# Performance work log

Measured on AMD Instinct MI355X. Metric: run time of the kernel, lower is better.

The kernel has to match this reference:

```python
import jax, jax.numpy as jnp
import numpy as np

GATE_INIT_BIAS = -0.6931471805599453  # -log(2)

def mish(x):
    return x * jnp.tanh(jax.nn.softplus(x))

def setup_inputs() -> dict:
    key = jax.random.key(0)
    ks = jax.random.split(key, 24)
    B = 262144
    x = jax.random.normal(ks[0], (B, 18), dtype=jnp.float32)
    band = jax.random.randint(ks[1], (B,), 0, 9).astype(jnp.float32)
    x = x.at[:, 17].set(band)
    def lin(k, fan_in, shape):
        bound = 1.0 / np.sqrt(fan_in)
        return jax.random.uniform(k, shape, jnp.float32, -bound, bound)
    inp = {
        'x': x,
        # trunk: 15->512->256 (Mish)
        'tw1': lin(ks[2], 15, (15, 512)),  'tb1': lin(ks[3], 15, (512,)),
        'tw2': lin(ks[4], 512, (512, 256)), 'tb2': lin(ks[5], 512, (256,)),
        # 9 band heads: 256->128->1, stacked on leading axis
        'hw1': lin(ks[6], 256, (9, 256, 128)), 'hb1': lin(ks[7], 256, (9, 128)),
        'hw2': lin(ks[8], 128, (9, 128)),      'hb2': lin(ks[9], 128, (9,)),
        # sun scaler head 256->64->1 (final layer zero weight, bias = gate_init_bias)
        'sw1': lin(ks[10], 256, (256, 64)), 'sb1': lin(ks[11], 256, (64,)),
        'sw2': jnp.zeros((64, 1), jnp.float32), 'sb2': jnp.full((1,), GATE_INIT_BIAS, jnp.float32),
        # storm scaler head
        'stw1': lin(ks[12], 256, (256, 64)), 'stb1': lin(ks[13], 256, (64,)),
        'stw2': jnp.zeros((64, 1), jnp.float32), 'stb2': jnp.full((1,), GATE_INIT_BIAS, jnp.float32),
        # monotonic sidecars: 1->8->1, softplus-positivized weights
        'sun_w1': lin(ks[14], 1, (1, 8)),  'sun_b1': lin(ks[15], 1, (8,)),
        'sun_w2': lin(ks[16], 8, (8, 1)),  'sun_b2': lin(ks[17], 8, (1,)),
        'storm_w1': lin(ks[18], 1, (1, 8)), 'storm_b1': lin(ks[19], 1, (8,)),
        'storm_w2': lin(ks[20], 8, (8, 1)), 'storm_b2': lin(ks[21], 8, (1,)),
    }
    return inp

def monotonic_mlp(v, w1, b1, w2, b2):
    # MonotonicMLP: positivity via softplus on weights, tanh hidden activation
    h = jnp.tanh(v @ jax.nn.softplus(w1) + b1)
    return h @ jax.nn.softplus(w2) + b2  # [B,1]

def reference(x, tw1, tb1, tw2, tb2, hw1, hb1, hw2, hb2,
              sw1, sb1, sw2, sb2, stw1, stb1, stw2, stb2,
              sun_w1, sun_b1, sun_w2, sun_b2,
              storm_w1, storm_b1, storm_w2, storm_b2):
    x_deep = x[:, :15]
    x_sfi = x[:, 15:16]
    x_kp = x[:, 16:17]
    band = x[:, 17].astype(jnp.int32)  # [B]

    # trunk
    t = mish(mish(x_deep @ tw1 + tb1) @ tw2 + tb2)  # [B,256]

    # all 9 band heads densely (faithful to original), then gather
    hh = mish(jnp.einsum('bd,kdh->bkh', t, hw1) + hb1)       # [B,9,128]
    all_heads = jnp.einsum('bkh,kh->bk', hh, hw2) + hb2      # [B,9]
    base_snr = jnp.take_along_axis(all_heads, band[:, None], axis=1)  # [B,1]

    sun_logit = mish(t @ sw1 + sb1) @ sw2 + sb2      # [B,1]
    storm_logit = mish(t @ stw1 + stb1) @ stw2 + stb2
    sun_gate = jax.nn.sigmoid(sun_logit)
    storm_gate = jax.nn.sigmoid(storm_logit)

    return base_snr + sun_gate * monotonic_mlp(x_sfi, sun_w1, sun_b1, sun_w2, sun_b2) \
                    + storm_gate * monotonic_mlp(x_kp, storm_w1, storm_b1, storm_w2, storm_b2)
```

## Files before the change

### kernel.cpp

```cpp
#include <hip/hip_runtime.h>
#include <cstdint>

typedef unsigned short u16;
typedef unsigned char u8;
typedef __attribute__((ext_vector_type(8))) __bf16 bf16x8;
typedef __attribute__((ext_vector_type(4))) float f32x4;

#define MFMA16(a, b, c) __builtin_amdgcn_mfma_f32_16x16x32_bf16((a), (b), (c), 0, 0, 0)

__device__ __forceinline__ u16 f2b(float f) {
    union { float f; unsigned u; } v; v.f = f;
    unsigned r = v.u + 0x7fffu + ((v.u >> 16) & 1u);
    return (u16)(r >> 16);
}
__device__ __forceinline__ u16 f2b_hw(float f) {
    union { __bf16 h; u16 u; } cv; cv.h = (__bf16)f; return cv.u;
}
__device__ __forceinline__ float b2f(u16 h) {
    union { unsigned u; float f; } v; v.u = ((unsigned)h) << 16; return v.f;
}
__device__ __forceinline__ float fast_rcp(float x) { return __builtin_amdgcn_rcpf(x); }
__device__ __forceinline__ float mish_f(float x) {
    float s = __expf(fminf(x, 40.0f));
    float p = s * (s + 2.0f);
    return x * p * fast_rcp(p + 2.0f);
}
__device__ __forceinline__ float tanh_f(float y) {
    float e = __expf(2.0f * y);
    return 1.0f - 2.0f * fast_rcp(e + 1.0f);
}
__device__ __forceinline__ float sigmoid_f(float y) {
    return fast_rcp(1.0f + __expf(-y));
}
__device__ __forceinline__ float splus(float w) { return log1pf(__expf(w)); }

__device__ __forceinline__ int swz(int row, int col) {
    return col ^ (((row >> 2) & 3) << 3);
}

template <int CTRL>
__device__ __forceinline__ float dpp_add(float v) {
    union { float f; int i; } s, p;
    s.f = v;
    p.i = __builtin_amdgcn_update_dpp(0, s.i, CTRL, 0xf, 0xf, true);
    return v + p.f;
}
__device__ __forceinline__ float row16_sum(float v) {
    v = dpp_add<0xB1>(v);
    v = dpp_add<0x4E>(v);
    v = dpp_add<0x141>(v);
    v = dpp_add<0x140>(v);
    return v;
}

#define WS_PERM      0u
#define WS_CNT       1179648u
#define WS_SP        1183744u
#define WS_W1P       1184768u
#define WS_W2F       1217536u
#define WS_HW1F      1479680u
#define WS_SWF       2069504u
#define WS_STWF      2102272u
#define WS_NEEDED    2135040u

#define CAPH 16384
#define REG_BLOCKS 256


__global__ __launch_bounds__(512) void k_pack(const float* __restrict__ x, int B,
                       const float* __restrict__ tw1, const float* __restrict__ tw2,
                       const float* __restrict__ hw1,
                       const float* __restrict__ sw1, const float* __restrict__ stw1,
                       const float* __restrict__ sun_w1, const float* __restrict__ sun_w2,
                       const float* __restrict__ storm_w1, const float* __restrict__ storm_w2,
                       u16* __restrict__ W1p, u16* __restrict__ W2f, u16* __restrict__ HWf,
                       u16* __restrict__ SWf, u16* __restrict__ STWf,
                       float* __restrict__ sp, int* __restrict__ cnt,
                       int* __restrict__ perm)
{
    __shared__ int wcnt[8][9];
    __shared__ int wpre[8][9];
    __shared__ int bbase[9];
    __shared__ u8 bL[512];
    const int tid  = threadIdx.x;
    const int lane = tid & 63, wave = tid >> 6;
    const int sub  = blockIdx.x & 1;
    const int i    = blockIdx.x * 512 + tid;

    {
        const size_t ebase = (size_t)blockIdx.x * 512 * 18;
        const float2* xs = (const float2*)(x + ebase);
        const size_t etotal = (size_t)B * 18;
        for (int p = tid; p < 4608; p += 512) {
            if (ebase + (size_t)p * 2 + 1 < etotal) {
                float2 v = xs[p];
                int e0 = p * 2;
                int r0 = e0 / 18, c0 = e0 - r0 * 18;
                if (c0 == 16) bL[r0] = (u8)(int)v.y;
            }
        }
    }
    __syncthreads();

    int band = -1, rank = 0;
    if (i < B) band = (int)bL[tid];
    for (int k = 0; k < 9; ++k) {
        unsigned long long m = __ballot(band == k);
        if (band == k) rank = __popcll(m & ((1ull << lane) - 1ull));
        if (lane == 0) wcnt[wave][k] = __popcll(m);
    }
    __syncthreads();
    if (tid < 9) {
        int run = 0;
        for (int w = 0; w < 8; ++w) { wpre[w][tid] = run; run += wcnt[w][tid]; }
        bbase[tid] = atomicAdd(&cnt[(tid * 2 + sub) * 32], run);
    }
    __syncthreads();
    if (band >= 0)
        perm[(band * 2 + sub) * CAPH + bbase[band] + wpre[wave][band] + rank] = i;

    const int gtid = blockIdx.x * 512 + tid;
    if (gtid < 32) {
        const float* srcs[4] = { sun_w1, sun_w2, storm_w1, storm_w2 };
        float w = srcs[gtid >> 3][gtid & 7];
        sp[gtid] = splus(w);
    }
    const int total = 16384 + 131072 + 294912 + 16384 + 16384;
    for (int i2 = gtid; i2 < total; i2 += 512 * 512) {
        int idx = i2;
        if (idx < 16384) {
            int n = idx >> 5, k = idx & 31;
            W1p[idx] = (k < 15) ? f2b(tw1[k * 512 + n]) : (u16)0;
        } else if ((idx -= 16384) < 131072) {
            int tile = idx >> 9, within = idx & 511;
            int lane2 = within >> 3, j = within & 7;
            int nt = tile >> 4, kb = tile & 15;
            int n = nt * 16 + (lane2 & 15);
            int k = kb * 32 + (lane2 >> 4) * 8 + j;
            W2f[idx] = f2b(tw2[k * 256 + n]);
        } else if ((idx -= 131072) < 294912) {
            int g = idx >> 15, r = idx & 32767;
            int tile = r >> 9, within = r & 511;
            int lane2 = within >> 3, j = within & 7;
            int nt = tile >> 3, kb = tile & 7;
            int n = nt * 16 + (lane2 & 15);
            int k = kb * 32 + (lane2 >> 4) * 8 + j;
            HWf[idx] = f2b(hw1[(g * 256 + k) * 128 + n]);
        } else if ((idx -= 294912) < 16384) {
            int tile = idx >> 9, within = idx & 511;
            int lane2 = within >> 3, j = within & 7;
            int nt = tile >> 3, kb = tile & 7;
            int n = nt * 16 + (lane2 & 15);
            int k = kb * 32 + (lane2 >> 4) * 8 + j;
            SWf[idx] = f2b(sw1[k * 64 + n]);
        } else {
            idx -= 16384;
            int tile = idx >> 9, within = idx & 511;
            int lane2 = within >> 3, j = within & 7;
            int nt = tile >> 3, kb = tile & 7;
            int n = nt * 16 + (lane2 & 15);
            int k = kb * 32 + (lane2 >> 4) * 8 + j;
            STWf[idx] = f2b(stw1[k * 64 + n]);
        }
    }
}

__global__ __launch_bounds__(512, 4) void k_main(
                       const float* __restrict__ x,
                       const int* __restrict__ perm,
                       const int* __restrict__ cnt,
                       const u16* __restrict__ W1p, const u16* __restrict__ W2f,
                       const u16* __restrict__ HWf,
                       const u16* __restrict__ SWf, const u16* __restrict__ STWf,
                       const float* __restrict__ tb1, const float* __restrict__ tb2,
                       const float* __restrict__ hb1, const float* __restrict__ hw2,
                       const float* __restrict__ hb2,
                       const float* __restrict__ sb1, const float* __restrict__ sw2,
                       const float* __restrict__ sb2,
                       const float* __restrict__ stb1, const float* __restrict__ stw2,
                       const float* __restrict__ stb2,
                       const float* __restrict__ sp,
                       const float* __restrict__ sun_b1, const float* __restrict__ sun_b2,
                       const float* __restrict__ storm_b1, const float* __restrict__ storm_b2,
                       float* __restrict__ out)
{
    const int region = blockIdx.x >> 8;
    const int loc    = blockIdx.x & 255;
    const int bb     = region >> 1;
    const int nr0    = cnt[region * 32] - loc * 64;
    if (nr0 <= 0) return;
    const int nrows  = nr0 > 64 ? 64 : nr0;
    const int rstart = region * CAPH + loc * 64;

    __shared__ union {
        u16 xA[64][32];
        float red[16][64];
    } su;
    __shared__ int rowsL[64];
    __shared__ float sfiL[64], kpL[64];
    __shared__ u16 buf[2][64][136];

    int tid = threadIdx.x;
    int lane = tid & 63, wave = tid >> 6;
    int quad = lane >> 4, l15 = lane & 15;

    if (tid < 64) {
        int r = rstart + (tid < nrows ? tid : 0);
        rowsL[tid] = perm[r];
    }
    for (int i = tid; i < 64 * 32; i += 512) ((u16*)su.xA)[i] = 0;
    __syncthreads();
    for (int i = tid; i < 64 * 18; i += 512) {
        int r = i / 18, c = i - r * 18;
        float v = x[rowsL[r] * 18 + c];
        if (c < 15) su.xA[r][c] = f2b_hw(v);
        else if (c == 15) sfiL[r] = v;
        else if (c == 16) kpL[r] = v;
    }
    __syncthreads();

    bf16x8 ax[4];
#pragma unroll
    for (int mt = 0; mt < 4; ++mt)
        ax[mt] = *(const bf16x8*)&su.xA[mt * 16 + l15][quad * 8];

    f32x4 acc2[2][4] = {};

    for (int c = 0; c < 4; ++c) {
        f32x4 acc1[4] = {};
        {
            int ncol = c * 128 + wave * 16 + l15;
            bf16x8 bw = *(const bf16x8*)&W1p[ncol * 32 + quad * 8];
#pragma unroll
            for (int mt = 0; mt < 4; ++mt)
                acc1[mt] = MFMA16(ax[mt], bw, acc1[mt]);
        }
        u16 (*bufc)[136] = buf[c & 1];
        {
            int ccol = wave * 16 + l15;
            float bias = tb1[c * 128 + ccol];
#pragma unroll
            for (int mt = 0; mt < 4; ++mt)
#pragma unroll
                for (int r = 0; r < 4; ++r) {
                    int rr = mt * 16 + quad * 4 + r;
                    bufc[rr][swz(rr, ccol)] = f2b_hw(mish_f(acc1[mt][r] + bias));
                }
        }
        __syncthreads();
        for (int ks = 0; ks < 4; ++ks) {
            bf16x8 a2[4];
#pragma unroll
            for (int mt = 0; mt < 4; ++mt) {
                int rr = mt * 16 + l15;
                a2[mt] = *(const bf16x8*)&bufc[rr][swz(rr, ks * 32 + quad * 8)];
            }
            int kb = c * 4 + ks;
#pragma unroll
            for (int ntl = 0; ntl < 2; ++ntl) {
                int nt = wave * 2 + ntl;
                bf16x8 bw = *(const bf16x8*)&W2f[((nt * 16 + kb) << 9) + lane * 8];
#pragma unroll
                for (int mt = 0; mt < 4; ++mt)
                    acc2[ntl][mt] = MFMA16(a2[mt], bw, acc2[ntl][mt]);
            }
        }
    }
    __syncthreads();

    u16 (*tmat)[264] = (u16(*)[264])buf;
#pragma unroll
    for (int ntl = 0; ntl < 2; ++ntl) {
        int col = wave * 32 + ntl * 16 + l15;
        float bias = tb2[col];
#pragma unroll
        for (int mt = 0; mt < 4; ++mt)
#pragma unroll
            for (int r = 0; r < 4; ++r) {
                int rr = mt * 16 + quad * 4 + r;
                tmat[rr][swz(rr, col)] = f2b_hw(mish_f(acc2[ntl][mt][r] + bias));
            }
    }
    __syncthreads();

    f32x4 acch[4] = {}, accg[4] = {};
    const u16* Hw = HWf + bb * 32768;
    const u16* Gw = (wave < 4) ? SWf : STWf;
    int gnt = wave & 3;
    for (int kb = 0; kb < 8; ++kb) {
        bf16x8 a3[4];
#pragma unroll
        for (int mt = 0; mt < 4; ++mt) {
            int rr = mt * 16 + l15;
            a3[mt] = *(const bf16x8*)&tmat[rr][swz(rr, kb * 32 + quad * 8)];
        }
        bf16x8 bh = *(const bf16x8*)&Hw[((wave * 8 + kb) << 9) + lane * 8];
        bf16x8 bg = *(const bf16x8*)&Gw[((gnt * 8 + kb) << 9) + lane * 8];
#pragma unroll
        for (int mt = 0; mt < 4; ++mt) {
            acch[mt] = MFMA16(a3[mt], bh, acch[mt]);
            accg[mt] = MFMA16(a3[mt], bg, accg[mt]);
        }
    }

    float hsum[4][4];
    {
        int col = wave * 16 + l15;
        float hb = hb1[bb * 128 + col];
        float wv = hw2[bb * 128 + col];
#pragma unroll
        for (int mt = 0; mt < 4; ++mt)
#pragma unroll
            for (int r = 0; r < 4; ++r)
                hsum[mt][r] = mish_f(acch[mt][r] + hb) * wv;
    }
    float gsum[4][4];
    {
        int n = gnt * 16 + l15;
        float gb = (wave < 4) ? sb1[n] : stb1[n];
        float gw = (wave < 4) ? sw2[n] : stw2[n];
#pragma unroll
        for (int mt = 0; mt < 4; ++mt)
#pragma unroll
            for (int r = 0; r < 4; ++r)
                gsum[mt][r] = mish_f(accg[mt][r] + gb) * gw;
    }
#pragma unroll
    for (int mt = 0; mt < 4; ++mt)
#pragma unroll
        for (int r = 0; r < 4; ++r) {
            hsum[mt][r] = row16_sum(hsum[mt][r]);
            gsum[mt][r] = row16_sum(gsum[mt][r]);
        }
    if (l15 == 0)
#pragma unroll
        for (int mt = 0; mt < 4; ++mt)
#pragma unroll
            for (int r = 0; r < 4; ++r) {
                int row = mt * 16 + quad * 4 + r;
                su.red[wave][row] = hsum[mt][r];
                su.red[8 + wave][row] = gsum[mt][r];
            }
    __syncthreads();

    if (tid < 64 && tid < nrows) {
        int row = tid;
        float head = hb2[bb];
#pragma unroll
        for (int w = 0; w < 8; ++w) head += su.red[w][row];
        float sl = sb2[0], tl = stb2[0];
#pragma unroll
        for (int w = 0; w < 4; ++w) { sl += su.red[8 + w][row]; tl += su.red[12 + w][row]; }
        float sg = sigmoid_f(sl);
        float tg = sigmoid_f(tl);
        float v1 = sfiL[row], v2 = kpL[row];
        float sun_val = sun_b2[0], storm_val = storm_b2[0];
#pragma unroll
        for (int j = 0; j < 8; ++j) {
            sun_val   += tanh_f(v1 * sp[j]      + sun_b1[j])   * sp[8 + j];
            storm_val += tanh_f(v2 * sp[16 + j] + storm_b1[j]) * sp[24 + j];
        }
        out[rowsL[row]] = head + sg * sun_val + tg * storm_val;
    }
}

__global__ __launch_bounds__(64) void k_simple(
    const float* __restrict__ x,
    const float* __restrict__ tw1, const float* __restrict__ tb1,
    const float* __restrict__ tw2, const float* __restrict__ tb2,
    const float* __restrict__ hw1, const float* __restrict__ hb1,
    const float* __restrict__ hw2, const float* __restrict__ hb2,
    const float* __restrict__ sw1, const float* __restrict__ sb1,
    const float* __restrict__ sw2, const float* __restrict__ sb2,
    const float* __restrict__ stw1, const float* __restrict__ stb1,
    const float* __restrict__ stw2, const float* __restrict__ stb2,
    const float* __restrict__ sun_w1, const float* __restrict__ sun_b1,
    const float* __restrict__ sun_w2, const float* __restrict__ sun_b2,
    const float* __restrict__ storm_w1, const float* __restrict__ storm_b1,
    const float* __restrict__ storm_w2, const float* __restrict__ storm_b2,
    float* __restrict__ out)
{
    __shared__ u16 t_lds[256 * 64];

    const int lane = threadIdx.x;
    const int r = blockIdx.x * 64 + lane;

    float xr[15];
#pragma unroll
    for (int k = 0; k < 15; ++k) xr[k] = x[r * 18 + k];
    const float sfi = x[r * 18 + 15];
    const float kp  = x[r * 18 + 16];
    const int band  = (int)x[r * 18 + 17];

    for (int tc = 0; tc < 4; ++tc) {
        float acc[64];
#pragma unroll
        for (int j = 0; j < 64; ++j) acc[j] = 0.0f;
        for (int n = 0; n < 512; ++n) {
            float p = tb1[n];
#pragma unroll
            for (int k = 0; k < 15; ++k) p += xr[k] * tw1[k * 512 + n];
            const float a1n = mish_f(p);
            const float* w2 = &tw2[n * 256 + tc * 64];
#pragma unroll
            for (int j = 0; j < 64; ++j) acc[j] += a1n * w2[j];
        }
#pragma unroll
        for (int j = 0; j < 64; ++j)
            t_lds[(tc * 64 + j) * 64 + lane] = f2b(mish_f(acc[j] + tb2[tc * 64 + j]));
    }
    __syncthreads();

    float head_val = 0.0f;
    for (int g = 0; g < 9; ++g) {
        float hs = 0.0f;
        for (int hc = 0; hc < 2; ++hc) {
            float pre[64];
#pragma unroll
            for (int j = 0; j < 64; ++j) pre[j] = 0.0f;
            for (int d = 0; d < 256; ++d) {
                const float td = b2f(t_lds[d * 64 + lane]);
                const float* wv = &hw1[g * 32768 + d * 128 + hc * 64];
#pragma unroll
                for (int j = 0; j < 64; ++j) pre[j] += td * wv[j];
            }
#pragma unroll
            for (int j = 0; j < 64; ++j) {
                const int h = hc * 64 + j;
                hs += mish_f(pre[j] + hb1[g * 128 + h]) * hw2[g * 128 + h];
            }
        }
        head_val += (band == g) ? (hs + hb2[g]) : 0.0f;
    }

    float pre_s[64], pre_t[64];
#pragma unroll
    for (int j = 0; j < 64; ++j) { pre_s[j] = 0.0f; pre_t[j] = 0.0f; }
    for (int d = 0; d < 256; ++d) {
        const float td = b2f(t_lds[d * 64 + lane]);
        const float* ws1 = &sw1[d * 64];
        const float* wt1 = &stw1[d * 64];
#pragma unroll
        for (int j = 0; j < 64; ++j) {
            pre_s[j] += td * ws1[j];
            pre_t[j] += td * wt1[j];
        }
    }
    float ls = sb2[0], lt = stb2[0];
#pragma unroll
    for (int j = 0; j < 64; ++j) {
        ls += mish_f(pre_s[j] + sb1[j]) * sw2[j];
        lt += mish_f(pre_t[j] + stb1[j]) * stw2[j];
    }
    const float sg = sigmoid_f(ls);
    const float tg = sigmoid_f(lt);

    float sun_val = sun_b2[0], storm_val = storm_b2[0];
#pragma unroll
    for (int j = 0; j < 8; ++j) {
        sun_val   += tanh_f(sfi * splus(sun_w1[j])  + sun_b1[j])   * splus(sun_w2[j]);
        storm_val += tanh_f(kp * splus(storm_w1[j]) + storm_b1[j]) * splus(storm_w2[j]);
    }

    out[r] = head_val + sg * sun_val + tg * storm_val;
}

extern "C" void kernel_launch(void* const* d_in, const int* in_sizes, int n_in,
                              void* d_out, int out_size, void* d_ws, size_t ws_size,
                              hipStream_t stream) {
    (void)n_in; (void)out_size;
    const float* x        = (const float*)d_in[0];
    const float* tw1      = (const float*)d_in[1];
    const float* tb1      = (const float*)d_in[2];
    const float* tw2      = (const float*)d_in[3];
    const float* tb2      = (const float*)d_in[4];
    const float* hw1      = (const float*)d_in[5];
    const float* hb1      = (const float*)d_in[6];
    const float* hw2      = (const float*)d_in[7];
    const float* hb2      = (const float*)d_in[8];
    const float* sw1      = (const float*)d_in[9];
    const float* sb1      = (const float*)d_in[10];
    const float* sw2      = (const float*)d_in[11];
    const float* sb2      = (const float*)d_in[12];
    const float* stw1     = (const float*)d_in[13];
    const float* stb1     = (const float*)d_in[14];
    const float* stw2     = (const float*)d_in[15];
    const float* stb2     = (const float*)d_in[16];
    const float* sun_w1   = (const float*)d_in[17];
    const float* sun_b1   = (const float*)d_in[18];
    const float* sun_w2   = (const float*)d_in[19];
    const float* sun_b2   = (const float*)d_in[20];
    const float* storm_w1 = (const float*)d_in[21];
    const float* storm_b1 = (const float*)d_in[22];
    const float* storm_w2 = (const float*)d_in[23];
    const float* storm_b2 = (const float*)d_in[24];

    const int B = in_sizes[0] / 18;

    if (ws_size < (size_t)WS_NEEDED) {
        k_simple<<<B / 64, 64, 0, stream>>>(x, tw1, tb1, tw2, tb2, hw1, hb1, hw2, hb2,
                                            sw1, sb1, sw2, sb2, stw1, stb1, stw2, stb2,
                                            sun_w1, sun_b1, sun_w2, sun_b2,
                                            storm_w1, storm_b1, storm_w2, storm_b2,
                                            (float*)d_out);
        return;
    }

    char* ws = (char*)d_ws;
    int*   perm      = (int*)(ws + WS_PERM);
    int*   cnt       = (int*)(ws + WS_CNT);
    float* sp        = (float*)(ws + WS_SP);
    u16*   W1p       = (u16*)(ws + WS_W1P);
    u16*   W2f       = (u16*)(ws + WS_W2F);
    u16*   HWf       = (u16*)(ws + WS_HW1F);
    u16*   SWf       = (u16*)(ws + WS_SWF);
    u16*   STWf      = (u16*)(ws + WS_STWF);

    hipMemsetAsync(cnt, 0, 18 * 32 * sizeof(int), stream);
    k_pack<<<(B + 511) / 512, 512, 0, stream>>>(x, B, tw1, tw2, hw1, sw1, stw1,
                                                sun_w1, sun_w2, storm_w1, storm_w2,
                                                W1p, W2f, HWf, SWf, STWf, sp, cnt, perm);
    k_main<<<18 * REG_BLOCKS, 512, 0, stream>>>(x, perm, cnt,
                                                W1p, W2f, HWf, SWf, STWf,
                                                tb1, tb2, hb1, hw2, hb2,
                                                sb1, sw2, sb2, stb1, stw2, stb2,
                                                sp, sun_b1, sun_b2, storm_b1, storm_b2,
                                                (float*)d_out);
}
```

Measured before the change: 315.8 us.

## Swap MFMA operand order to transpose outputs and vectorize epilogues

Swaps the A/B operands of every MFMA so each lane holds four consecutive output columns for one row instead of four rows of one column. The epilogues can then load biases as float4, pack results with v_cvt_pk_bf16_f32, and write 8-byte vector stores to LDS without the XOR swizzle. The head reductions become in-register sums plus two cross-quad shuffles, replacing the 16-element DPP row reductions. The risk is LDS bank conflicts on the now unswizzled row-major reads and writes.

```diff
diff --git a/kernel.cpp b/kernel.cpp
--- a/kernel.cpp
+++ b/kernel.cpp
@@ -5,6 +5,7 @@
 typedef unsigned char u8;
 typedef __attribute__((ext_vector_type(8))) __bf16 bf16x8;
 typedef __attribute__((ext_vector_type(4))) float f32x4;
+typedef __attribute__((ext_vector_type(2))) unsigned u32x2;
 
 #define MFMA16(a, b, c) __builtin_amdgcn_mfma_f32_16x16x32_bf16((a), (b), (c), 0, 0, 0)
 
@@ -18,6 +19,11 @@
 }
 __device__ __forceinline__ float b2f(u16 h) {
     union { unsigned u; float f; } v; v.u = ((unsigned)h) << 16; return v.f;
+}
+__device__ __forceinline__ unsigned cvt_pk_bf16(float lo, float hi) {
+    unsigned r;
+    asm("v_cvt_pk_bf16_f32 %0, %1, %2" : "=v"(r) : "v"(lo), "v"(hi));
+    return r;
 }
 __device__ __forceinline__ float fast_rcp(float x) { return __builtin_amdgcn_rcpf(x); }
 __device__ __forceinline__ float mish_f(float x) {
@@ -34,9 +40,6 @@
 }
 __device__ __forceinline__ float splus(float w) { return log1pf(__expf(w)); }
 
-__device__ __forceinline__ int swz(int row, int col) {
-    return col ^ (((row >> 2) & 3) << 3);
-}
 
 template <int CTRL>
 __device__ __forceinline__ float dpp_add(float v) {
@@ -44,13 +47,6 @@
     s.f = v;
     p.i = __builtin_amdgcn_update_dpp(0, s.i, CTRL, 0xf, 0xf, true);
     return v + p.f;
-}
-__device__ __forceinline__ float row16_sum(float v) {
-    v = dpp_add<0xB1>(v);
-    v = dpp_add<0x4E>(v);
-    v = dpp_add<0x141>(v);
-    v = dpp_add<0x140>(v);
-    return v;
 }
 
 #define WS_PERM      0u
@@ -233,28 +229,27 @@
             bf16x8 bw = *(const bf16x8*)&W1p[ncol * 32 + quad * 8];
 #pragma unroll
             for (int mt = 0; mt < 4; ++mt)
-                acc1[mt] = MFMA16(ax[mt], bw, acc1[mt]);
+                acc1[mt] = MFMA16(bw, ax[mt], acc1[mt]);
         }
         u16 (*bufc)[136] = buf[c & 1];
         {
-            int ccol = wave * 16 + l15;
-            float bias = tb1[c * 128 + ccol];
-#pragma unroll
-            for (int mt = 0; mt < 4; ++mt)
-#pragma unroll
-                for (int r = 0; r < 4; ++r) {
-                    int rr = mt * 16 + quad * 4 + r;
-                    bufc[rr][swz(rr, ccol)] = f2b_hw(mish_f(acc1[mt][r] + bias));
-                }
+            const f32x4 bias = *(const f32x4*)&tb1[c * 128 + wave * 16 + quad * 4];
+#pragma unroll
+            for (int mt = 0; mt < 4; ++mt) {
+                u32x2 pk;
+                pk.x = cvt_pk_bf16(mish_f(acc1[mt][0] + bias[0]),
+                                   mish_f(acc1[mt][1] + bias[1]));
+                pk.y = cvt_pk_bf16(mish_f(acc1[mt][2] + bias[2]),
+                                   mish_f(acc1[mt][3] + bias[3]));
+                *(u32x2*)&bufc[mt * 16 + l15][wave * 16 + quad * 4] = pk;
+            }
         }
         __syncthreads();
         for (int ks = 0; ks < 4; ++ks) {
             bf16x8 a2[4];
 #pragma unroll
-            for (int mt = 0; mt < 4; ++mt) {
-                int rr = mt * 16 + l15;
-                a2[mt] = *(const bf16x8*)&bufc[rr][swz(rr, ks * 32 + quad * 8)];
-            }
+            for (int mt = 0; mt < 4; ++mt)
+                a2[mt] = *(const bf16x8*)&bufc[mt * 16 + l15][ks * 32 + quad * 8];
             int kb = c * 4 + ks;
 #pragma unroll
             for (int ntl = 0; ntl < 2; ++ntl) {
@@ -262,7 +257,7 @@
                 bf16x8 bw = *(const bf16x8*)&W2f[((nt * 16 + kb) << 9) + lane * 8];
 #pragma unroll
                 for (int mt = 0; mt < 4; ++mt)
-                    acc2[ntl][mt] = MFMA16(a2[mt], bw, acc2[ntl][mt]);
+                    acc2[ntl][mt] = MFMA16(bw, a2[mt], acc2[ntl][mt]);
             }
         }
     }
@@ -271,15 +266,17 @@
     u16 (*tmat)[264] = (u16(*)[264])buf;
 #pragma unroll
     for (int ntl = 0; ntl < 2; ++ntl) {
-        int col = wave * 32 + ntl * 16 + l15;
-        float bias = tb2[col];
-#pragma unroll
-        for (int mt = 0; mt < 4; ++mt)
-#pragma unroll
-            for (int r = 0; r < 4; ++r) {
-                int rr = mt * 16 + quad * 4 + r;
-                tmat[rr][swz(rr, col)] = f2b_hw(mish_f(acc2[ntl][mt][r] + bias));
-            }
+        const int colb = wave * 32 + ntl * 16 + quad * 4;
+        const f32x4 bias = *(const f32x4*)&tb2[colb];
+#pragma unroll
+        for (int mt = 0; mt < 4; ++mt) {
+            u32x2 pk;
+            pk.x = cvt_pk_bf16(mish_f(acc2[ntl][mt][0] + bias[0]),
+                               mish_f(acc2[ntl][mt][1] + bias[1]));
+            pk.y = cvt_pk_bf16(mish_f(acc2[ntl][mt][2] + bias[2]),
+                               mish_f(acc2[ntl][mt][3] + bias[3]));
+            *(u32x2*)&tmat[mt * 16 + l15][colb] = pk;
+        }
     }
     __syncthreads();
 
@@ -290,57 +287,54 @@
     for (int kb = 0; kb < 8; ++kb) {
         bf16x8 a3[4];
 #pragma unroll
-        for (int mt = 0; mt < 4; ++mt) {
-            int rr = mt * 16 + l15;
-            a3[mt] = *(const bf16x8*)&tmat[rr][swz(rr, kb * 32 + quad * 8)];
-        }
+        for (int mt = 0; mt < 4; ++mt)
+            a3[mt] = *(const bf16x8*)&tmat[mt * 16 + l15][kb * 32 + quad * 8];
         bf16x8 bh = *(const bf16x8*)&Hw[((wave * 8 + kb) << 9) + lane * 8];
         bf16x8 bg = *(const bf16x8*)&Gw[((gnt * 8 + kb) << 9) + lane * 8];
 #pragma unroll
         for (int mt = 0; mt < 4; ++mt) {
-            acch[mt] = MFMA16(a3[mt], bh, acch[mt]);
-            accg[mt] = MFMA16(a3[mt], bg, accg[mt]);
-        }
-    }
-
-    float hsum[4][4];
+            acch[mt] = MFMA16(bh, a3[mt], acch[mt]);
+            accg[mt] = MFMA16(bg, a3[mt], accg[mt]);
+        }
+    }
+
+    float hpart[4], gpart[4];
     {
-        int col = wave * 16 + l15;
-        float hb = hb1[bb * 128 + col];
-        float wv = hw2[bb * 128 + col];
-#pragma unroll
-        for (int mt = 0; mt < 4; ++mt)
-#pragma unroll
-            for (int r = 0; r < 4; ++r)
-                hsum[mt][r] = mish_f(acch[mt][r] + hb) * wv;
-    }
-    float gsum[4][4];
+        const int colb = wave * 16 + quad * 4;
+        const f32x4 hb = *(const f32x4*)&hb1[bb * 128 + colb];
+        const f32x4 wv = *(const f32x4*)&hw2[bb * 128 + colb];
+#pragma unroll
+        for (int mt = 0; mt < 4; ++mt) {
+            float s = mish_f(acch[mt][0] + hb[0]) * wv[0];
+            s += mish_f(acch[mt][1] + hb[1]) * wv[1];
+            s += mish_f(acch[mt][2] + hb[2]) * wv[2];
+            s += mish_f(acch[mt][3] + hb[3]) * wv[3];
+            hpart[mt] = s;
+        }
+    }
     {
-        int n = gnt * 16 + l15;
-        float gb = (wave < 4) ? sb1[n] : stb1[n];
-        float gw = (wave < 4) ? sw2[n] : stw2[n];
-#pragma unroll
-        for (int mt = 0; mt < 4; ++mt)
-#pragma unroll
-            for (int r = 0; r < 4; ++r)
-                gsum[mt][r] = mish_f(accg[mt][r] + gb) * gw;
-    }
-#pragma unroll
-    for (int mt = 0; mt < 4; ++mt)
-#pragma unroll
-        for (int r = 0; r < 4; ++r) {
-            hsum[mt][r] = row16_sum(hsum[mt][r]);
-            gsum[mt][r] = row16_sum(gsum[mt][r]);
-        }
-    if (l15 == 0)
-#pragma unroll
-        for (int mt = 0; mt < 4; ++mt)
-#pragma unroll
-            for (int r = 0; r < 4; ++r) {
-                int row = mt * 16 + quad * 4 + r;
-                su.red[wave][row] = hsum[mt][r];
-                su.red[8 + wave][row] = gsum[mt][r];
-            }
+        const int nb = gnt * 16 + quad * 4;
+        const f32x4 gb = (wave < 4) ? *(const f32x4*)&sb1[nb] : *(const f32x4*)&stb1[nb];
+        const f32x4 gw = (wave < 4) ? *(const f32x4*)&sw2[nb] : *(const f32x4*)&stw2[nb];
+#pragma unroll
+        for (int mt = 0; mt < 4; ++mt) {
+            float s = mish_f(accg[mt][0] + gb[0]) * gw[0];
+            s += mish_f(accg[mt][1] + gb[1]) * gw[1];
+            s += mish_f(accg[mt][2] + gb[2]) * gw[2];
+            s += mish_f(accg[mt][3] + gb[3]) * gw[3];
+            gpart[mt] = s;
+        }
+    }
+#pragma unroll
+    for (int mt = 0; mt < 4; ++mt) {
+        float h = hpart[mt], g = gpart[mt];
+        h += __shfl_xor(h, 16); h += __shfl_xor(h, 32);
+        g += __shfl_xor(g, 16); g += __shfl_xor(g, 32);
+        if (quad == 0) {
+            su.red[wave][mt * 16 + l15] = h;
+            su.red[8 + wave][mt * 16 + l15] = g;
+        }
+    }
     __syncthreads();
 
     if (tid < 64 && tid < nrows) {
```

New measurement: 296.2 us. -6.2%, faster.
